# Kernel tuning notes

Hardware: AMD Instinct MI355X
Metric: run time of the kernel (lower is better)

The kernel has to match this reference:

```python
import jax, jax.numpy as jnp
import numpy as np

BETA = 0.95   # snn.Leaky(beta=0.95)
UTH = 1.0     # threshold from init_kwargs


def setup_inputs() -> dict:
    key = jax.random.key(0)
    N, T = 8192, 4000
    inp = jax.random.uniform(key, (N, T), dtype=jnp.float32)
    return {"inp": inp}


def reference(inp):
    # snntorch Leaky recurrence (reset_mechanism='subtract'):
    #   reset_t = H(mem_{t-1} - uth)            (uses PREVIOUS membrane)
    #   mem_t   = beta*mem_{t-1} + x_t - reset_t*uth
    #   spk_t   = H(mem_t - uth)
    # with mem_0 = 0. Outputs stacked spikes [N, T].
    dtype = inp.dtype
    uth = jnp.asarray(UTH, dtype)

    def step(mem, x):
        reset = (mem > uth).astype(dtype)
        mem_new = BETA * mem + x - reset * uth
        spk = (mem_new > uth).astype(dtype)
        return mem_new, spk

    mem0 = jnp.zeros(inp.shape[0], dtype=dtype)
    _, spikes_tn = jax.lax.scan(step, mem0, inp.T)  # [T, N]
    return spikes_tn.T  # [N, T]
```

## Files before the change

### kernel.cpp

```cpp
#include <hip/hip_runtime.h>


namespace {

constexpr int T_LEN = 4000;
constexpr int N_NEU = 8192;
constexpr int QROW  = 128;
constexpr size_t QBYTES = (size_t)N_NEU * QROW * 4;

__device__ __forceinline__ unsigned step1(float x, float& mem, float& r) {
    float t = __fmul_rn(0.95f, mem);
    t       = __fadd_rn(t, x);
    mem     = __fsub_rn(t, r);
    bool s  = mem > 1.0f;
    r = s ? 1.0f : 0.0f;
    return s ? 1u : 0u;
}

template <int PF>
__device__ __forceinline__ void half16(const float* __restrict__ p,
                                       float4* __restrict__ ring,
                                       float& mem, float& r,
                                       unsigned& u0, unsigned& u1) {
    u0 = 0; u1 = 0;
#pragma unroll
    for (int j = 0; j < 16; ++j) {
        float4 v = ring[j];
        if (j < PF)
            ring[j] = *reinterpret_cast<const float4*>(p + 64 + 4 * j);
        unsigned b;
        b  = step1(v.x, mem, r);
        b |= step1(v.y, mem, r) << 1;
        b |= step1(v.z, mem, r) << 2;
        b |= step1(v.w, mem, r) << 3;
        const unsigned sh = (j & 7) * 4;
        if (j < 8) u0 |= b << sh; else u1 |= b << sh;
    }
    __builtin_amdgcn_sched_barrier(0);
}

__global__ __launch_bounds__(64, 1)
void snn_scan(const float* __restrict__ x, unsigned* __restrict__ q) {
    const int l = threadIdx.x;
    const size_t n = (size_t)blockIdx.x * 64 + l;
    const float* p = x + n * T_LEN;
    unsigned* qn = q + n * QROW;

    float mem = 0.0f;
    float r   = 0.0f;

    float4 ring[16];
#pragma unroll
    for (int j = 0; j < 16; ++j)
        ring[j] = *reinterpret_cast<const float4*>(p + 4 * j);

    unsigned w0, w1, w2, w3;
#pragma unroll 1
    for (int k = 0; k < 30; ++k) {
        half16<16>(p,      ring, mem, r, w0, w1);
        half16<16>(p + 64, ring, mem, r, w2, w3);
        *reinterpret_cast<uint4*>(qn) = make_uint4(w0, w1, w2, w3);
        qn += 4;
        p  += 128;
    }
    half16<16>(p,      ring, mem, r, w0, w1);
    half16<8 >(p + 64, ring, mem, r, w2, w3);
    *reinterpret_cast<uint4*>(qn) = make_uint4(w0, w1, w2, w3);
    unsigned u = 0;
#pragma unroll
    for (int j = 0; j < 8; ++j) {
        float4 v = ring[j];
        unsigned b;
        b  = step1(v.x, mem, r);
        b |= step1(v.y, mem, r) << 1;
        b |= step1(v.z, mem, r) << 2;
        b |= step1(v.w, mem, r) << 3;
        u |= b << (j * 4);
    }
    qn[4] = u;
}

__global__ __launch_bounds__(256)
void snn_expand(const unsigned* __restrict__ q, float* __restrict__ out) {
    const unsigned i = blockIdx.x * 256 + threadIdx.x;
    const unsigned n = i / 1000u;
    const unsigned c = i - n * 1000u;
    const unsigned w = q[n * QROW + (c >> 3)];
    const unsigned nib = w >> ((c & 7u) * 4u);
    float4 f;
    f.x = (nib & 1u) ? 1.0f : 0.0f;
    f.y = (nib & 2u) ? 1.0f : 0.0f;
    f.z = (nib & 4u) ? 1.0f : 0.0f;
    f.w = (nib & 8u) ? 1.0f : 0.0f;
    reinterpret_cast<float4*>(out)[i] = f;
}

}

extern "C" void kernel_launch(void* const* d_in, const int* in_sizes, int n_in,
                              void* d_out, int out_size, void* d_ws, size_t ws_size,
                              hipStream_t stream) {
    const float* x = (const float*)d_in[0];
    float* out     = (float*)d_out;
    unsigned* q    = (unsigned*)d_ws;
    snn_scan<<<dim3(N_NEU / 64), dim3(64), 0, stream>>>(x, q);
    snn_expand<<<dim3(32000), dim3(256), 0, stream>>>(q, out);
}
```

Before: 258.9 us.

## Split each neuron across four lanes with DPP broadcast for coalesced input loads

The scan kernel now assigns each neuron to a quad of four lanes. Each lane loads an interleaved float4 chunk so that the quad together reads contiguous 64-byte segments, and DPP quad-permute broadcasts the values so every lane runs the same serial recurrence redundantly. Spike bits are packed with an FMA accumulator instead of integer shifts and ORs, and only the lead lane writes. The aim is better load coalescing and four times as many wavefronts to hide memory latency. The cost is four-fold redundant compute and extra DPP moves on the serial dependency chain.

```diff
diff --git a/kernel.cpp b/kernel.cpp
--- a/kernel.cpp
+++ b/kernel.cpp
@@ -6,78 +6,107 @@
 constexpr int T_LEN = 4000;
 constexpr int N_NEU = 8192;
 constexpr int QROW  = 128;
-constexpr size_t QBYTES = (size_t)N_NEU * QROW * 4;
 
-__device__ __forceinline__ unsigned step1(float x, float& mem, float& r) {
+__device__ __forceinline__ void stepf(float xv, float& mem, float& r,
+                                      float& acc, float bit) {
     float t = __fmul_rn(0.95f, mem);
-    t       = __fadd_rn(t, x);
+    t       = __fadd_rn(t, xv);
     mem     = __fsub_rn(t, r);
     bool s  = mem > 1.0f;
-    r = s ? 1.0f : 0.0f;
-    return s ? 1u : 0u;
+    r   = s ? 1.0f : 0.0f;
+    acc = __fmaf_rn(r, bit, acc);
 }
 
-template <int PF>
-__device__ __forceinline__ void half16(const float* __restrict__ p,
-                                       float4* __restrict__ ring,
-                                       float& mem, float& r,
-                                       unsigned& u0, unsigned& u1) {
-    u0 = 0; u1 = 0;
-#pragma unroll
-    for (int j = 0; j < 16; ++j) {
-        float4 v = ring[j];
-        if (j < PF)
-            ring[j] = *reinterpret_cast<const float4*>(p + 64 + 4 * j);
-        unsigned b;
-        b  = step1(v.x, mem, r);
-        b |= step1(v.y, mem, r) << 1;
-        b |= step1(v.z, mem, r) << 2;
-        b |= step1(v.w, mem, r) << 3;
-        const unsigned sh = (j & 7) * 4;
-        if (j < 8) u0 |= b << sh; else u1 |= b << sh;
-    }
+template<int J>
+__device__ __forceinline__ float qb(float v) {
+    return __int_as_float(
+        __builtin_amdgcn_mov_dpp(__float_as_int(v), J * 0x55, 0xF, 0xF, true));
+}
+template<int J>
+__device__ __forceinline__ float4 qb4(const float4 v) {
+    float4 o;
+    o.x = qb<J>(v.x); o.y = qb<J>(v.y); o.z = qb<J>(v.z); o.w = qb<J>(v.w);
+    return o;
+}
+
+template<int SLOT, bool REFILL>
+__device__ __forceinline__ unsigned group16(const float* __restrict__ p,
+                                            float4* __restrict__ ring,
+                                            float& mem, float& r) {
+    float4 a0 = qb4<0>(ring[SLOT]);
+    float4 a1 = qb4<1>(ring[SLOT]);
+    float4 a2 = qb4<2>(ring[SLOT]);
+    float4 a3 = qb4<3>(ring[SLOT]);
+    if (REFILL)
+        ring[SLOT] = *reinterpret_cast<const float4*>(p + 128 + 16 * SLOT);
+    float acc = 0.0f;
+    stepf(a0.x, mem, r, acc, 1.f);      stepf(a0.y, mem, r, acc, 2.f);
+    stepf(a0.z, mem, r, acc, 4.f);      stepf(a0.w, mem, r, acc, 8.f);
+    stepf(a1.x, mem, r, acc, 16.f);     stepf(a1.y, mem, r, acc, 32.f);
+    stepf(a1.z, mem, r, acc, 64.f);     stepf(a1.w, mem, r, acc, 128.f);
+    stepf(a2.x, mem, r, acc, 256.f);    stepf(a2.y, mem, r, acc, 512.f);
+    stepf(a2.z, mem, r, acc, 1024.f);   stepf(a2.w, mem, r, acc, 2048.f);
+    stepf(a3.x, mem, r, acc, 4096.f);   stepf(a3.y, mem, r, acc, 8192.f);
+    stepf(a3.z, mem, r, acc, 16384.f);  stepf(a3.w, mem, r, acc, 32768.f);
     __builtin_amdgcn_sched_barrier(0);
+    return (unsigned)acc;
 }
 
 __global__ __launch_bounds__(64, 1)
 void snn_scan(const float* __restrict__ x, unsigned* __restrict__ q) {
-    const int l = threadIdx.x;
-    const size_t n = (size_t)blockIdx.x * 64 + l;
-    const float* p = x + n * T_LEN;
-    unsigned* qn = q + n * QROW;
+    const int l    = threadIdx.x;
+    const int j    = l & 3;
+    const int n    = blockIdx.x * 16 + (l >> 2);
+    const bool lead = (j == 0);
+
+    const float* p = x + (size_t)n * T_LEN + 4 * j;
+    unsigned* qn   = q + (size_t)n * QROW;
 
     float mem = 0.0f;
     float r   = 0.0f;
 
-    float4 ring[16];
+    float4 ring[8];
 #pragma unroll
-    for (int j = 0; j < 16; ++j)
-        ring[j] = *reinterpret_cast<const float4*>(p + 4 * j);
+    for (int i = 0; i < 8; ++i)
+        ring[i] = *reinterpret_cast<const float4*>(p + 16 * i);
 
-    unsigned w0, w1, w2, w3;
 #pragma unroll 1
     for (int k = 0; k < 30; ++k) {
-        half16<16>(p,      ring, mem, r, w0, w1);
-        half16<16>(p + 64, ring, mem, r, w2, w3);
-        *reinterpret_cast<uint4*>(qn) = make_uint4(w0, w1, w2, w3);
+        unsigned u0 = group16<0, true>(p, ring, mem, r);
+        unsigned u1 = group16<1, true>(p, ring, mem, r);
+        unsigned u2 = group16<2, true>(p, ring, mem, r);
+        unsigned u3 = group16<3, true>(p, ring, mem, r);
+        unsigned u4 = group16<4, true>(p, ring, mem, r);
+        unsigned u5 = group16<5, true>(p, ring, mem, r);
+        unsigned u6 = group16<6, true>(p, ring, mem, r);
+        unsigned u7 = group16<7, true>(p, ring, mem, r);
+        if (lead)
+            *reinterpret_cast<uint4*>(qn) =
+                make_uint4(u0 | (u1 << 16), u2 | (u3 << 16),
+                           u4 | (u5 << 16), u6 | (u7 << 16));
         qn += 4;
         p  += 128;
     }
-    half16<16>(p,      ring, mem, r, w0, w1);
-    half16<8 >(p + 64, ring, mem, r, w2, w3);
-    *reinterpret_cast<uint4*>(qn) = make_uint4(w0, w1, w2, w3);
-    unsigned u = 0;
-#pragma unroll
-    for (int j = 0; j < 8; ++j) {
-        float4 v = ring[j];
-        unsigned b;
-        b  = step1(v.x, mem, r);
-        b |= step1(v.y, mem, r) << 1;
-        b |= step1(v.z, mem, r) << 2;
-        b |= step1(v.w, mem, r) << 3;
-        u |= b << (j * 4);
+    {
+        unsigned u0 = group16<0, true >(p, ring, mem, r);
+        unsigned u1 = group16<1, true >(p, ring, mem, r);
+        unsigned u2 = group16<2, false>(p, ring, mem, r);
+        unsigned u3 = group16<3, false>(p, ring, mem, r);
+        unsigned u4 = group16<4, false>(p, ring, mem, r);
+        unsigned u5 = group16<5, false>(p, ring, mem, r);
+        unsigned u6 = group16<6, false>(p, ring, mem, r);
+        unsigned u7 = group16<7, false>(p, ring, mem, r);
+        if (lead)
+            *reinterpret_cast<uint4*>(qn) =
+                make_uint4(u0 | (u1 << 16), u2 | (u3 << 16),
+                           u4 | (u5 << 16), u6 | (u7 << 16));
+        qn += 4;
+        p  += 128;
     }
-    qn[4] = u;
+    unsigned e0 = group16<0, false>(p, ring, mem, r);
+    unsigned e1 = group16<1, false>(p, ring, mem, r);
+    if (lead)
+        qn[0] = e0 | (e1 << 16);
 }
 
 __global__ __launch_bounds__(256)
@@ -103,6 +132,6 @@
     const float* x = (const float*)d_in[0];
     float* out     = (float*)d_out;
     unsigned* q    = (unsigned*)d_ws;
-    snn_scan<<<dim3(N_NEU / 64), dim3(64), 0, stream>>>(x, q);
+    snn_scan<<<dim3(N_NEU / 16), dim3(64), 0, stream>>>(x, q);
     snn_expand<<<dim3(32000), dim3(256), 0, stream>>>(q, out);
 }
```

Measured after the change: 236.9 us, median of 2. -8.5%, faster.
